# Performance work log

Hardware: AMD Instinct MI355X
Metric: run time of the kernel (lower is better)

## Reference

```python
import jax, jax.numpy as jnp
import numpy as np

N_FFT = 1024
HOP = 256
BATCH = 16
SAMPLES = 262144


def hann_window(n):
    # torch.hann_window default (periodic=True): 0.5 * (1 - cos(2*pi*k/n))
    k = jnp.arange(n, dtype=jnp.float32)
    return 0.5 - 0.5 * jnp.cos(2.0 * jnp.pi * k / n)


def setup_inputs() -> dict:
    key = jax.random.key(0)
    x = jax.random.normal(key, (BATCH, SAMPLES), dtype=jnp.float32)
    window = hann_window(N_FFT)  # (n_fft,)
    return {"x": x, "window": window}


def reference(x, window):
    # Faithful STFT.forward: pad -> frame (identity-kernel conv1d == gather) ->
    # window -> rfft along the frame axis; norm=None.
    pad = N_FFT - HOP
    pad_left = pad // 2
    xp = jnp.pad(x, ((0, 0), (pad_left, pad - pad_left)))
    n_frames = (xp.shape[1] - N_FFT) // HOP + 1
    # gather-based framing, equivalent to conv1d with eye(n_fft) kernel, stride=hop
    idx = jnp.arange(n_frames)[:, None] * HOP + jnp.arange(N_FFT)[None, :]  # (frames, n_fft)
    frames = xp[:, idx]                       # (B, frames, n_fft)
    frames = frames * window[None, None, :]   # windowing
    spec = jnp.fft.rfft(frames, axis=-1)      # (B, frames, n_bins)
    real = jnp.transpose(spec.real, (0, 2, 1))  # (B, n_bins, frames)
    imag = jnp.transpose(spec.imag, (0, 2, 1))
    return real, imag
```

## Files before the change

kernel.cpp:

```cpp
#include <hip/hip_runtime.h>

#define HOP      256
#define SAMPLES  262144
#define NBINS    513
#define NFRAMES  1024
#define FPB      16

typedef float v2f __attribute__((ext_vector_type(2)));

__device__ __forceinline__ v2f nI(v2f a) { v2f r = a.yx; r.y = -r.y; return r; }

__device__ __forceinline__ v2f cmul2(v2f a, v2f b) {
  v2f bs = b.yx; bs.x = -bs.x;
  return a.xx * b + a.yy * bs;
}

__device__ __forceinline__ v2f lds_ld(const v2f* p, int bo) {
  return *(const v2f*)((const char*)p + bo);
}
__device__ __forceinline__ void lds_st(v2f* p, int bo, v2f v) {
  *(v2f*)((char*)p + bo) = v;
}
__device__ __forceinline__ int swz(int c) {
  int H = c >> 6, M = (c >> 3) & 7, L = c & 7;
  return (H << 6) | ((M ^ (H & 1)) << 3) | (L ^ M);
}

__device__ __forceinline__ void fft8(v2f v[8]) {
  const float R = 0.70710678118654752440f;
  v2f s0 = v[0] + v[4], d0 = v[0] - v[4];
  v2f s1 = v[1] + v[5], d1 = v[1] - v[5];
  v2f s2 = v[2] + v[6], d2 = v[2] - v[6];
  v2f s3 = v[3] + v[7], d3 = v[3] - v[7];
  v2f e1 = R * (d1 + nI(d1));
  v2f e2 = nI(d2);
  v2f e3 = R * (nI(d3) - d3);
  v2f p0 = s0 + s2, q0 = s0 - s2;
  v2f p1 = s1 + s3, q1 = s1 - s3;
  v2f q1t = nI(q1);
  v2f p2 = d0 + e2, q2 = d0 - e2;
  v2f p3 = e1 + e3, q3 = e1 - e3;
  v2f q3t = nI(q3);
  v[0] = p0 + p1;  v[4] = p0 - p1;
  v[2] = q0 + q1t; v[6] = q0 - q1t;
  v[1] = p2 + p3;  v[5] = p2 - p3;
  v[3] = q2 + q3t; v[7] = q2 - q3t;
}

#define UNPK(ZP, KEY, SK, SM, TW, X1, D) {                           \
    v2f Zk = lds_ld(ZP, ((SK) ^ (KEY)) << 3);                        \
    v2f Zm = lds_ld(ZP, ((SM) ^ (KEY)) << 3);                        \
    v2f mc = Zm; mc.y = -mc.y;                                       \
    v2f xe = Zk + mc;                                                \
    v2f xo = nI(Zk) + Zm.yx;                                         \
    v2f u  = cmul2(TW, xo);                                          \
    X1 = xe + u; D = xe - u; }

__global__ __launch_bounds__(1024, 8)
void stft_kernel(const float* __restrict__ x, const float* __restrict__ win,
                 float* __restrict__ out) {
  __shared__ v2f z[FPB * 512];
  __shared__ v2f T1[7][64];
  __shared__ v2f T2[7][8];
  __shared__ v2f TU[256];
  __shared__ float WH[1024];

  const int t  = threadIdx.x;
  const int b  = blockIdx.x >> 6;
  const int f0 = (blockIdx.x & 63) * FPB;
  const int w  = t >> 6;
  const int u  = t & 63;
  const int g  = u >> 3, m2l = u & 7;

  const float* xb = x + (size_t)b * SAMPLES;
  const int base = (f0 + w) * HOP - 384;
  v2f r[8];
  if (f0 != 0 && f0 != (NFRAMES - FPB)) {
    const v2f* xc = (const v2f*)(xb + base);
#pragma unroll
    for (int n1 = 0; n1 < 8; ++n1) r[n1] = xc[(n1 << 6) + u];
  } else {
#pragma unroll
    for (int n1 = 0; n1 < 8; ++n1) {
      int idx = base + (n1 << 7) + 2 * u;
      r[n1] = (v2f){0.f, 0.f};
      if (idx >= 0 && idx < SAMPLES) r[n1] = *(const v2f*)(xb + idx);
    }
  }

  {
    WH[t] = 0.5f * win[t];
    float sn, cs;
    if (t < 448) {
      int k = t >> 6, uu = t & 63;
      __sincosf((float)(uu * (k + 1)) * (-6.28318530717958647693f / 512.f),
                &sn, &cs);
      T1[k][uu] = (v2f){cs, sn};
    } else if (t < 504) {
      int i = t - 448, k = i >> 3, m = i & 7;
      __sincosf((float)(m * (k + 1)) * (-6.28318530717958647693f / 64.f),
                &sn, &cs);
      T2[k][m] = (v2f){cs, sn};
    } else if (t >= 512 && t < 768) {
      int kk = t - 512;
      __sincosf((float)kk * (-6.28318530717958647693f / 1024.f), &sn, &cs);
      TU[kk] = (v2f){cs, sn};
    }
  }
  __syncthreads();

  {
    v2f* zf = z + (w << 9);
    const int A0    = (g << 3) | (m2l ^ g);
    const int B1w_e = (A0 ^ w) << 3;
    const int B1w_o = B1w_e ^ 64;
    const int C1    = (g << 6) | ((g & 1) << 3) | m2l;
    const int B1r   = (C1 ^ w) << 3;
    const int D0    = (g << 6) | ((m2l ^ (g & 1)) << 3) | m2l;
    const int B2r   = (D0 ^ w) << 3;
    const int F0    = (m2l << 3) | (g ^ m2l);
    const int B3_e  = (F0 ^ w) << 3;
    const int B3_o  = B3_e ^ 64;

    const v2f* wh2 = (const v2f*)WH;
#pragma unroll
    for (int n1 = 0; n1 < 8; ++n1) r[n1] = r[n1] * wh2[(n1 << 6) + u];

    fft8(r);
#pragma unroll
    for (int k = 1; k < 8; ++k) r[k] = cmul2(r[k], T1[k - 1][u]);
    lds_st(zf, B1w_e,        r[0]);
    lds_st(zf, B1w_o +  512, r[1]);
    lds_st(zf, B1w_e + 1024, r[2]);
    lds_st(zf, B1w_o + 1536, r[3]);
    lds_st(zf, B1w_e + 2048, r[4]);
    lds_st(zf, B1w_o + 2560, r[5]);
    lds_st(zf, B1w_e + 3072, r[6]);
    lds_st(zf, B1w_o + 3584, r[7]);

    v2f y[8];
#pragma unroll
    for (int m1 = 0; m1 < 8; ++m1) y[m1] = lds_ld(zf, B1r ^ (72 * m1));

    fft8(y);
#pragma unroll
    for (int k = 1; k < 8; ++k) y[k] = cmul2(y[k], T2[k - 1][m2l]);
#pragma unroll
    for (int j1 = 0; j1 < 8; ++j1) lds_st(zf, B1r ^ (72 * j1), y[j1]);

    v2f h[8];
#pragma unroll
    for (int m = 0; m < 8; ++m) h[m] = lds_ld(zf, B2r ^ (m << 3));

    fft8(h);
    lds_st(zf, B3_e,        h[0]);
    lds_st(zf, B3_o +  512, h[1]);
    lds_st(zf, B3_e + 1024, h[2]);
    lds_st(zf, B3_o + 1536, h[3]);
    lds_st(zf, B3_e + 2048, h[4]);
    lds_st(zf, B3_o + 2560, h[5]);
    lds_st(zf, B3_e + 3072, h[6]);
    lds_st(zf, B3_o + 3584, h[7]);
  }
  __syncthreads();

  {
    const int f2i = t & 7;
    const int q   = t >> 3;
    const int f   = f2i << 1;
    const int fr  = f0 + f;
    const v2f* zp0 = z + (f << 9);
    const v2f* zp1 = z + ((f + 1) << 9);

    const int sk0 = swz(q);
    const int sm0 = swz((512 - q) & 511);
    const int sk1 = sk0 + 128;
    const int sm1 = (q == 0) ? 384 : (sm0 - 128);

    const v2f tw0 = TU[q];
    const v2f tw1 = TU[q + 128];
    float* out_r = out;
    float* out_i = out + (size_t)16 * NBINS * NFRAMES;
    const size_t o1 = ((size_t)b * NBINS + q) * NFRAMES + fr;
    const size_t o2 = ((size_t)b * NBINS + (512 - q)) * NFRAMES + fr;
    const size_t STP = (size_t)128 * NFRAMES;

    {
      v2f X1a, Da, X1b, Db;
      UNPK(zp0, f,     sk0, sm0, tw0, X1a, Da)
      UNPK(zp1, f + 1, sk0, sm0, tw0, X1b, Db)
      *(v2f*)(out_r + o1) = (v2f){X1a.x, X1b.x};
      *(v2f*)(out_i + o1) = (v2f){X1a.y, X1b.y};
      *(v2f*)(out_r + o2) = (v2f){Da.x, Db.x};
      *(v2f*)(out_i + o2) = (v2f){-Da.y, -Db.y};
    }
    {
      v2f X1a, Da, X1b, Db;
      UNPK(zp0, f,     sk1, sm1, tw1, X1a, Da)
      UNPK(zp1, f + 1, sk1, sm1, tw1, X1b, Db)
      *(v2f*)(out_r + o1 + STP) = (v2f){X1a.x, X1b.x};
      *(v2f*)(out_i + o1 + STP) = (v2f){X1a.y, X1b.y};
      *(v2f*)(out_r + o2 - STP) = (v2f){Da.x, Db.x};
      *(v2f*)(out_i + o2 - STP) = (v2f){-Da.y, -Db.y};
    }
    if (q == 0) {
      v2f Za = lds_ld(zp0, (256 ^ f) << 3);
      v2f Zb = lds_ld(zp1, (256 ^ (f + 1)) << 3);
      const size_t o6 = ((size_t)b * NBINS + 256) * NFRAMES + fr;
      *(v2f*)(out_r + o6) = (v2f){Za.x + Za.x, Zb.x + Zb.x};
      *(v2f*)(out_i + o6) = (v2f){-(Za.y + Za.y), -(Zb.y + Zb.y)};
    }
  }
}

extern "C" void kernel_launch(void* const* d_in, const int* in_sizes, int n_in,
                              void* d_out, int out_size, void* d_ws, size_t ws_size,
                              hipStream_t stream) {
  const float* x = (const float*)d_in[0];
  const float* w = (const float*)d_in[1];
  float* out = (float*)d_out;
  (void)in_sizes; (void)n_in; (void)out_size; (void)d_ws; (void)ws_size;
  stft_kernel<<<dim3(1024), dim3(1024), 0, stream>>>(x, w, out);
}
```

Measured before the change: 23.93 us.

## Store FFT intermediates as fp16 in LDS and halve block threads

Intermediate FFT values in shared memory are now stored as packed fp16 pairs, converted with round-toward-zero, which halves the LDS footprint and traffic per frame. Each block now uses 512 threads, each handling two frames, and the window is read directly from global memory rather than staged in shared memory. The aim is to raise occupancy and cut LDS bandwidth. The cost is lost precision in the intermediates, which may exceed the tolerance on 1024-point transforms.

```diff
diff --git a/kernel.cpp b/kernel.cpp
--- a/kernel.cpp
+++ b/kernel.cpp
@@ -6,20 +6,21 @@
 #define NFRAMES  1024
 #define FPB      16
 
-typedef float v2f __attribute__((ext_vector_type(2)));
+typedef float  v2f __attribute__((ext_vector_type(2)));
+typedef __fp16 h2  __attribute__((ext_vector_type(2)));
 
 __device__ __forceinline__ v2f nI(v2f a) { v2f r = a.yx; r.y = -r.y; return r; }
-
 __device__ __forceinline__ v2f cmul2(v2f a, v2f b) {
   v2f bs = b.yx; bs.x = -bs.x;
   return a.xx * b + a.yy * bs;
 }
 
-__device__ __forceinline__ v2f lds_ld(const v2f* p, int bo) {
-  return *(const v2f*)((const char*)p + bo);
-}
-__device__ __forceinline__ void lds_st(v2f* p, int bo, v2f v) {
-  *(v2f*)((char*)p + bo) = v;
+__device__ __forceinline__ void lds_st16(h2* p, int bo, v2f v) {
+  *(h2*)((char*)p + bo) = __builtin_amdgcn_cvt_pkrtz(v.x, v.y);
+}
+__device__ __forceinline__ v2f lds_ld16(const h2* p, int bo) {
+  h2 h = *(const h2*)((const char*)p + bo);
+  return (v2f){(float)h.x, (float)h.y};
 }
 __device__ __forceinline__ int swz(int c) {
   int H = c >> 6, M = (c >> 3) & 7, L = c & 7;
@@ -47,120 +48,153 @@
   v[3] = q2 + q3t; v[7] = q2 - q3t;
 }
 
+#define FFT_S1(R, ZF, E1, O1) {                                          \
+    fft8(R);                                                             \
+    _Pragma("unroll")                                                    \
+    for (int k = 1; k < 8; ++k) R[k] = cmul2(R[k], T1[k - 1][u]);        \
+    lds_st16(ZF, (E1),        R[0]);                                     \
+    lds_st16(ZF, (O1) +  256, R[1]);                                     \
+    lds_st16(ZF, (E1) +  512, R[2]);                                     \
+    lds_st16(ZF, (O1) +  768, R[3]);                                     \
+    lds_st16(ZF, (E1) + 1024, R[4]);                                     \
+    lds_st16(ZF, (O1) + 1280, R[5]);                                     \
+    lds_st16(ZF, (E1) + 1536, R[6]);                                     \
+    lds_st16(ZF, (O1) + 1792, R[7]);                                     \
+  }
+
+#define FFT_S2(Y, ZF, BR) {                                              \
+    _Pragma("unroll")                                                    \
+    for (int m1 = 0; m1 < 8; ++m1) Y[m1] = lds_ld16(ZF, (BR) ^ (36*m1)); \
+    fft8(Y);                                                             \
+    _Pragma("unroll")                                                    \
+    for (int k = 1; k < 8; ++k) Y[k] = cmul2(Y[k], T2[k - 1][m2l]);      \
+    _Pragma("unroll")                                                    \
+    for (int j1 = 0; j1 < 8; ++j1) lds_st16(ZF, (BR) ^ (36*j1), Y[j1]);  \
+  }
+
+#define FFT_S3(H, ZF, B2, E3, O3) {                                      \
+    _Pragma("unroll")                                                    \
+    for (int m = 0; m < 8; ++m) H[m] = lds_ld16(ZF, (B2) ^ (m << 2));    \
+    fft8(H);                                                             \
+    lds_st16(ZF, (E3),        H[0]);                                     \
+    lds_st16(ZF, (O3) +  256, H[1]);                                     \
+    lds_st16(ZF, (E3) +  512, H[2]);                                     \
+    lds_st16(ZF, (O3) +  768, H[3]);                                     \
+    lds_st16(ZF, (E3) + 1024, H[4]);                                     \
+    lds_st16(ZF, (O3) + 1280, H[5]);                                     \
+    lds_st16(ZF, (E3) + 1536, H[6]);                                     \
+    lds_st16(ZF, (O3) + 1792, H[7]);                                     \
+  }
+
 #define UNPK(ZP, KEY, SK, SM, TW, X1, D) {                           \
-    v2f Zk = lds_ld(ZP, ((SK) ^ (KEY)) << 3);                        \
-    v2f Zm = lds_ld(ZP, ((SM) ^ (KEY)) << 3);                        \
+    v2f Zk = lds_ld16(ZP, ((SK) ^ (KEY)) << 2);                      \
+    v2f Zm = lds_ld16(ZP, ((SM) ^ (KEY)) << 2);                      \
     v2f mc = Zm; mc.y = -mc.y;                                       \
     v2f xe = Zk + mc;                                                \
     v2f xo = nI(Zk) + Zm.yx;                                         \
-    v2f u  = cmul2(TW, xo);                                          \
-    X1 = xe + u; D = xe - u; }
-
-__global__ __launch_bounds__(1024, 8)
+    v2f uu = cmul2(TW, xo);                                          \
+    X1 = xe + uu; D = xe - uu; }
+
+__global__ __launch_bounds__(512, 8)
 void stft_kernel(const float* __restrict__ x, const float* __restrict__ win,
                  float* __restrict__ out) {
-  __shared__ v2f z[FPB * 512];
+  __shared__ h2  z[FPB * 512];
   __shared__ v2f T1[7][64];
   __shared__ v2f T2[7][8];
   __shared__ v2f TU[256];
-  __shared__ float WH[1024];
 
   const int t  = threadIdx.x;
   const int b  = blockIdx.x >> 6;
   const int f0 = (blockIdx.x & 63) * FPB;
-  const int w  = t >> 6;
+  const int w2 = t >> 6;
   const int u  = t & 63;
   const int g  = u >> 3, m2l = u & 7;
 
   const float* xb = x + (size_t)b * SAMPLES;
-  const int base = (f0 + w) * HOP - 384;
-  v2f r[8];
-  if (f0 != 0 && f0 != (NFRAMES - FPB)) {
-    const v2f* xc = (const v2f*)(xb + base);
-#pragma unroll
-    for (int n1 = 0; n1 < 8; ++n1) r[n1] = xc[(n1 << 6) + u];
+  const int baseA = (f0 + w2) * HOP - 384;
+  const int baseB = baseA + 8 * HOP;
+  v2f ra[8], rb[8];
+  if (f0 != 0) {
+    const v2f* xc = (const v2f*)(xb + baseA);
+#pragma unroll
+    for (int n1 = 0; n1 < 8; ++n1) ra[n1] = xc[(n1 << 6) + u];
   } else {
 #pragma unroll
     for (int n1 = 0; n1 < 8; ++n1) {
-      int idx = base + (n1 << 7) + 2 * u;
-      r[n1] = (v2f){0.f, 0.f};
-      if (idx >= 0 && idx < SAMPLES) r[n1] = *(const v2f*)(xb + idx);
+      int idx = baseA + (n1 << 7) + 2 * u;
+      ra[n1] = (v2f){0.f, 0.f};
+      if (idx >= 0) ra[n1] = *(const v2f*)(xb + idx);
+    }
+  }
+  if (f0 != (NFRAMES - FPB)) {
+    const v2f* xc = (const v2f*)(xb + baseB);
+#pragma unroll
+    for (int n1 = 0; n1 < 8; ++n1) rb[n1] = xc[(n1 << 6) + u];
+  } else {
+#pragma unroll
+    for (int n1 = 0; n1 < 8; ++n1) {
+      int idx = baseB + (n1 << 7) + 2 * u;
+      rb[n1] = (v2f){0.f, 0.f};
+      if (idx < SAMPLES) rb[n1] = *(const v2f*)(xb + idx);
     }
   }
 
   {
-    WH[t] = 0.5f * win[t];
     float sn, cs;
     if (t < 448) {
-      int k = t >> 6, uu = t & 63;
-      __sincosf((float)(uu * (k + 1)) * (-6.28318530717958647693f / 512.f),
+      int k = t >> 6, uu2 = t & 63;
+      __sincosf((float)(uu2 * (k + 1)) * (-6.28318530717958647693f / 512.f),
                 &sn, &cs);
-      T1[k][uu] = (v2f){cs, sn};
+      T1[k][uu2] = (v2f){cs, sn};
     } else if (t < 504) {
       int i = t - 448, k = i >> 3, m = i & 7;
       __sincosf((float)(m * (k + 1)) * (-6.28318530717958647693f / 64.f),
                 &sn, &cs);
       T2[k][m] = (v2f){cs, sn};
-    } else if (t >= 512 && t < 768) {
-      int kk = t - 512;
-      __sincosf((float)kk * (-6.28318530717958647693f / 1024.f), &sn, &cs);
-      TU[kk] = (v2f){cs, sn};
+    }
+    if (t < 256) {
+      __sincosf((float)t * (-6.28318530717958647693f / 1024.f), &sn, &cs);
+      TU[t] = (v2f){cs, sn};
     }
   }
   __syncthreads();
 
   {
-    v2f* zf = z + (w << 9);
+    h2* zfA = z + (w2 << 9);
+    h2* zfB = z + ((w2 + 8) << 9);
     const int A0    = (g << 3) | (m2l ^ g);
-    const int B1w_e = (A0 ^ w) << 3;
-    const int B1w_o = B1w_e ^ 64;
+    const int B1w_e = (A0 ^ w2) << 2;
+    const int B1w_o = B1w_e ^ 32;
     const int C1    = (g << 6) | ((g & 1) << 3) | m2l;
-    const int B1r   = (C1 ^ w) << 3;
+    const int B1r   = (C1 ^ w2) << 2;
     const int D0    = (g << 6) | ((m2l ^ (g & 1)) << 3) | m2l;
-    const int B2r   = (D0 ^ w) << 3;
+    const int B2r   = (D0 ^ w2) << 2;
     const int F0    = (m2l << 3) | (g ^ m2l);
-    const int B3_e  = (F0 ^ w) << 3;
-    const int B3_o  = B3_e ^ 64;
-
-    const v2f* wh2 = (const v2f*)WH;
-#pragma unroll
-    for (int n1 = 0; n1 < 8; ++n1) r[n1] = r[n1] * wh2[(n1 << 6) + u];
-
-    fft8(r);
-#pragma unroll
-    for (int k = 1; k < 8; ++k) r[k] = cmul2(r[k], T1[k - 1][u]);
-    lds_st(zf, B1w_e,        r[0]);
-    lds_st(zf, B1w_o +  512, r[1]);
-    lds_st(zf, B1w_e + 1024, r[2]);
-    lds_st(zf, B1w_o + 1536, r[3]);
-    lds_st(zf, B1w_e + 2048, r[4]);
-    lds_st(zf, B1w_o + 2560, r[5]);
-    lds_st(zf, B1w_e + 3072, r[6]);
-    lds_st(zf, B1w_o + 3584, r[7]);
-
-    v2f y[8];
-#pragma unroll
-    for (int m1 = 0; m1 < 8; ++m1) y[m1] = lds_ld(zf, B1r ^ (72 * m1));
-
-    fft8(y);
-#pragma unroll
-    for (int k = 1; k < 8; ++k) y[k] = cmul2(y[k], T2[k - 1][m2l]);
-#pragma unroll
-    for (int j1 = 0; j1 < 8; ++j1) lds_st(zf, B1r ^ (72 * j1), y[j1]);
-
-    v2f h[8];
-#pragma unroll
-    for (int m = 0; m < 8; ++m) h[m] = lds_ld(zf, B2r ^ (m << 3));
-
-    fft8(h);
-    lds_st(zf, B3_e,        h[0]);
-    lds_st(zf, B3_o +  512, h[1]);
-    lds_st(zf, B3_e + 1024, h[2]);
-    lds_st(zf, B3_o + 1536, h[3]);
-    lds_st(zf, B3_e + 2048, h[4]);
-    lds_st(zf, B3_o + 2560, h[5]);
-    lds_st(zf, B3_e + 3072, h[6]);
-    lds_st(zf, B3_o + 3584, h[7]);
+    const int B3_e  = (F0 ^ w2) << 2;
+    const int B3_o  = B3_e ^ 32;
+
+    const v2f* wc = (const v2f*)win;
+#pragma unroll
+    for (int n1 = 0; n1 < 8; ++n1) {
+      v2f wv = wc[(n1 << 6) + u] * 0.5f;
+      ra[n1] = ra[n1] * wv;
+      rb[n1] = rb[n1] * wv;
+    }
+
+    FFT_S1(ra, zfA, B1w_e, B1w_o)
+    FFT_S1(rb, zfB, B1w_o, B1w_e)
+    {
+      v2f y[8];
+      FFT_S2(y, zfA, B1r)
+      v2f y2[8];
+      FFT_S2(y2, zfB, B1r ^ 32)
+    }
+    {
+      v2f h_[8];
+      FFT_S3(h_, zfA, B2r, B3_e, B3_o)
+      v2f h2_[8];
+      FFT_S3(h2_, zfB, B2r ^ 32, B3_o, B3_e)
+    }
   }
   __syncthreads();
 
@@ -169,43 +203,46 @@
     const int q   = t >> 3;
     const int f   = f2i << 1;
     const int fr  = f0 + f;
-    const v2f* zp0 = z + (f << 9);
-    const v2f* zp1 = z + ((f + 1) << 9);
-
-    const int sk0 = swz(q);
-    const int sm0 = swz((512 - q) & 511);
-    const int sk1 = sk0 + 128;
-    const int sm1 = (q == 0) ? 384 : (sm0 - 128);
-
-    const v2f tw0 = TU[q];
-    const v2f tw1 = TU[q + 128];
+    const h2* zp0 = z + (f << 9);
+    const h2* zp1 = z + ((f + 1) << 9);
     float* out_r = out;
     float* out_i = out + (size_t)16 * NBINS * NFRAMES;
-    const size_t o1 = ((size_t)b * NBINS + q) * NFRAMES + fr;
-    const size_t o2 = ((size_t)b * NBINS + (512 - q)) * NFRAMES + fr;
     const size_t STP = (size_t)128 * NFRAMES;
 
-    {
-      v2f X1a, Da, X1b, Db;
-      UNPK(zp0, f,     sk0, sm0, tw0, X1a, Da)
-      UNPK(zp1, f + 1, sk0, sm0, tw0, X1b, Db)
-      *(v2f*)(out_r + o1) = (v2f){X1a.x, X1b.x};
-      *(v2f*)(out_i + o1) = (v2f){X1a.y, X1b.y};
-      *(v2f*)(out_r + o2) = (v2f){Da.x, Db.x};
-      *(v2f*)(out_i + o2) = (v2f){-Da.y, -Db.y};
-    }
-    {
-      v2f X1a, Da, X1b, Db;
-      UNPK(zp0, f,     sk1, sm1, tw1, X1a, Da)
-      UNPK(zp1, f + 1, sk1, sm1, tw1, X1b, Db)
-      *(v2f*)(out_r + o1 + STP) = (v2f){X1a.x, X1b.x};
-      *(v2f*)(out_i + o1 + STP) = (v2f){X1a.y, X1b.y};
-      *(v2f*)(out_r + o2 - STP) = (v2f){Da.x, Db.x};
-      *(v2f*)(out_i + o2 - STP) = (v2f){-Da.y, -Db.y};
+#pragma unroll
+    for (int hh = 0; hh < 2; ++hh) {
+      const int qq  = q + (hh << 6);
+      const int sk0 = swz(qq);
+      const int sm0 = swz((512 - qq) & 511);
+      const int sk1 = sk0 + 128;
+      const int sm1 = (qq == 0) ? 384 : (sm0 - 128);
+      const v2f tw0 = TU[qq];
+      const v2f tw1 = TU[qq + 128];
+      const size_t o1 = ((size_t)b * NBINS + qq) * NFRAMES + fr;
+      const size_t o2 = ((size_t)b * NBINS + (512 - qq)) * NFRAMES + fr;
+
+      {
+        v2f X1a, Da, X1b, Db;
+        UNPK(zp0, f,     sk0, sm0, tw0, X1a, Da)
+        UNPK(zp1, f + 1, sk0, sm0, tw0, X1b, Db)
+        *(v2f*)(out_r + o1) = (v2f){X1a.x, X1b.x};
+        *(v2f*)(out_i + o1) = (v2f){X1a.y, X1b.y};
+        *(v2f*)(out_r + o2) = (v2f){Da.x, Db.x};
+        *(v2f*)(out_i + o2) = (v2f){-Da.y, -Db.y};
+      }
+      {
+        v2f X1a, Da, X1b, Db;
+        UNPK(zp0, f,     sk1, sm1, tw1, X1a, Da)
+        UNPK(zp1, f + 1, sk1, sm1, tw1, X1b, Db)
+        *(v2f*)(out_r + o1 + STP) = (v2f){X1a.x, X1b.x};
+        *(v2f*)(out_i + o1 + STP) = (v2f){X1a.y, X1b.y};
+        *(v2f*)(out_r + o2 - STP) = (v2f){Da.x, Db.x};
+        *(v2f*)(out_i + o2 - STP) = (v2f){-Da.y, -Db.y};
+      }
     }
     if (q == 0) {
-      v2f Za = lds_ld(zp0, (256 ^ f) << 3);
-      v2f Zb = lds_ld(zp1, (256 ^ (f + 1)) << 3);
+      v2f Za = lds_ld16(zp0, (256 ^ f) << 2);
+      v2f Zb = lds_ld16(zp1, (256 ^ (f + 1)) << 2);
       const size_t o6 = ((size_t)b * NBINS + 256) * NFRAMES + fr;
       *(v2f*)(out_r + o6) = (v2f){Za.x + Za.x, Zb.x + Zb.x};
       *(v2f*)(out_i + o6) = (v2f){-(Za.y + Za.y), -(Zb.y + Zb.y)};
@@ -220,5 +257,5 @@
   const float* w = (const float*)d_in[1];
   float* out = (float*)d_out;
   (void)in_sizes; (void)n_in; (void)out_size; (void)d_ws; (void)ws_size;
-  stft_kernel<<<dim3(1024), dim3(1024), 0, stream>>>(x, w, out);
-}
+  stft_kernel<<<dim3(1024), dim3(512), 0, stream>>>(x, w, out);
+}
```

After: 23.08 us, median of 2. -3.6%, faster.
